# Performance work log

Measured on AMD Instinct MI355X. Metric: run time of the kernel, lower is better.

The kernel has to match this reference:

```python
import jax, jax.numpy as jnp
import numpy as np

D = 512; H = 8; DFF = 2048; S1 = 1024; S2 = 512; B = 8; EPS = 1e-5


def setup_inputs() -> dict:
    key = jax.random.key(0)
    ks = jax.random.split(key, 10)
    def w(k, shape):
        return jax.random.normal(k, shape, dtype=jnp.float32) * 0.02
    return {
        "rna_embed": jax.random.normal(ks[0], (S1, B, D), dtype=jnp.float32),
        "protein_embed": jax.random.normal(ks[1], (S2, B, D), dtype=jnp.float32),
        # self-attention params (torch MHA packed in_proj)
        "Wqkv_s": w(ks[2], (3 * D, D)), "bqkv_s": jnp.zeros((3 * D,), jnp.float32),
        "Wo_s": w(ks[3], (D, D)), "bo_s": jnp.zeros((D,), jnp.float32),
        # cross-attention params
        "Wqkv_c": w(ks[4], (3 * D, D)), "bqkv_c": jnp.zeros((3 * D,), jnp.float32),
        "Wo_c": w(ks[5], (D, D)), "bo_c": jnp.zeros((D,), jnp.float32),
        # FFN params
        "W1": w(ks[6], (DFF, D)), "b1": jnp.zeros((DFF,), jnp.float32),
        "W2": w(ks[7], (D, DFF)), "b2": jnp.zeros((D,), jnp.float32),
        # LayerNorm params: norm0_1, norm1_1, norm1_2, norm2
        "g0": jnp.ones((D,), jnp.float32), "be0": jnp.zeros((D,), jnp.float32),
        "g11": jnp.ones((D,), jnp.float32), "be11": jnp.zeros((D,), jnp.float32),
        "g12": jnp.ones((D,), jnp.float32), "be12": jnp.zeros((D,), jnp.float32),
        "g2": jnp.ones((D,), jnp.float32), "be2": jnp.zeros((D,), jnp.float32),
    }


def _layernorm(x, g, b):
    m = jnp.mean(x, axis=-1, keepdims=True)
    v = jnp.mean(jnp.square(x - m), axis=-1, keepdims=True)
    return (x - m) * jax.lax.rsqrt(v + EPS) * g + b


def _mha(xq, xkv, Wqkv, bqkv, Wo, bo):
    # xq: (Sq, B, D), xkv: (Sk, B, D)
    Wq, Wk, Wv = jnp.split(Wqkv, 3, axis=0)
    bq, bk, bv = jnp.split(bqkv, 3)
    hd = D // H
    scale = 1.0 / np.sqrt(hd).astype(np.float32)
    q = (xq @ Wq.T + bq).reshape(xq.shape[0], -1, H, hd)   # (Sq,B,H,hd)
    k = (xkv @ Wk.T + bk).reshape(xkv.shape[0], -1, H, hd)  # (Sk,B,H,hd)
    v = (xkv @ Wv.T + bv).reshape(xkv.shape[0], -1, H, hd)
    scores = jnp.einsum('qbhd,kbhd->bhqk', q, k) * scale    # (B,H,Sq,Sk)
    attn = jax.nn.softmax(scores, axis=-1)
    o = jnp.einsum('bhqk,kbhd->qbhd', attn, v).reshape(xq.shape[0], -1, D)
    return o @ Wo.T + bo


def reference(rna_embed, protein_embed, Wqkv_s, bqkv_s, Wo_s, bo_s,
              Wqkv_c, bqkv_c, Wo_c, bo_c, W1, b1, W2, b2,
              g0, be0, g11, be11, g12, be12, g2, be2):
    x1 = rna_embed
    # pre-norm self-attention
    h = _layernorm(x1, g0, be0)
    x1 = x1 + _mha(h, h, Wqkv_s, bqkv_s, Wo_s, bo_s)
    # pre-norm cross-attention (queries from x1, keys/values from protein)
    x1 = x1 + _mha(_layernorm(x1, g11, be11), _layernorm(protein_embed, g12, be12),
                   Wqkv_c, bqkv_c, Wo_c, bo_c)
    # pre-norm FFN
    h = _layernorm(x1, g2, be2)
    x1 = x1 + (jax.nn.relu(h @ W1.T + b1) @ W2.T + b2)
    return x1
```

## Files before the change

### kernel.cpp

```cpp
#include <hip/hip_runtime.h>

typedef unsigned short u16;
typedef unsigned int u32;
typedef u16 u16x8 __attribute__((ext_vector_type(8)));
typedef u16 u16x4 __attribute__((ext_vector_type(4)));
typedef short bfx8 __attribute__((ext_vector_type(8)));
typedef float f32x4 __attribute__((ext_vector_type(4)));

#define AS1 __attribute__((address_space(1)))
#define AS3 __attribute__((address_space(3)))

__device__ __forceinline__ u16 f2bf(float f) {
  union { float f; u32 u; } c; c.f = f;
  u32 u = c.u;
  u += 0x7fffu + ((u >> 16) & 1u);
  return (u16)(u >> 16);
}

__device__ __forceinline__ float bf2f(u16 b) {
  union { u32 u; float f; } c; c.u = ((u32)b) << 16;
  return c.f;
}

__device__ __forceinline__ u32 cvt_pk_bf16(float lo, float hi) {
  u32 r;
  asm("v_cvt_pk_bf16_f32 %0, %1, %2" : "=v"(r) : "v"(lo), "v"(hi));
  return r;
}

__device__ __forceinline__ float fexp2(float x) {
  float r;
  asm("v_exp_f32 %0, %1" : "=v"(r) : "v"(x));
  return r;
}

__device__ __forceinline__ void ln_core(float f[8], const float* __restrict__ g,
                                        const float* __restrict__ be,
                                        u16* __restrict__ out, int gw, int lane) {
  float s = 0.f, q = 0.f;
#pragma unroll
  for (int e = 0; e < 8; ++e) { s += f[e]; q += f[e] * f[e]; }
#pragma unroll
  for (int m = 1; m < 64; m <<= 1) { s += __shfl_xor(s, m); q += __shfl_xor(q, m); }
  float mean = s * (1.f / 512.f);
  float var = q * (1.f / 512.f) - mean * mean;
  float rs = rsqrtf(var + 1e-5f);
  const float4* g4 = (const float4*)g;
  const float4* b4 = (const float4*)be;
  float4 ga = g4[2 * lane], gb = g4[2 * lane + 1];
  float4 ba = b4[2 * lane], bb = b4[2 * lane + 1];
  float gv[8] = {ga.x, ga.y, ga.z, ga.w, gb.x, gb.y, gb.z, gb.w};
  float bv[8] = {ba.x, ba.y, ba.z, ba.w, bb.x, bb.y, bb.z, bb.w};
  u16x8 o;
#pragma unroll
  for (int e = 0; e < 8; ++e) o[e] = f2bf((f[e] - mean) * rs * gv[e] + bv[e]);
  ((u16x8*)(out + (size_t)gw * 512))[lane] = o;
}

__device__ __forceinline__ void ln_row_f32(const float* __restrict__ x, const float* __restrict__ g,
                                           const float* __restrict__ be, u16* __restrict__ out,
                                           int gw, int lane) {
  const float4* row = (const float4*)(x + (size_t)gw * 512);
  float4 a = row[2 * lane], b = row[2 * lane + 1];
  float f[8] = {a.x, a.y, a.z, a.w, b.x, b.y, b.z, b.w};
  ln_core(f, g, be, out, gw, lane);
}

__device__ __forceinline__ void ln_row_bf16(const u16* __restrict__ x, const float* __restrict__ g,
                                            const float* __restrict__ be, u16* __restrict__ out,
                                            int gw, int lane) {
  u16x8 v = ((const u16x8*)(x + (size_t)gw * 512))[lane];
  float f[8];
#pragma unroll
  for (int e = 0; e < 8; ++e) f[e] = bf2f(v[e]);
  ln_core(f, g, be, out, gw, lane);
}

__global__ __launch_bounds__(256) void cvtln_kernel(const float* __restrict__ a0, const float* __restrict__ a1,
                                                    const float* __restrict__ a2, const float* __restrict__ a3,
                                                    const float* __restrict__ a4, const float* __restrict__ a5,
                                                    u16* __restrict__ b0, u16* __restrict__ b1,
                                                    u16* __restrict__ b2, u16* __restrict__ b3,
                                                    u16* __restrict__ b4, u16* __restrict__ b5,
                                                    const float* __restrict__ x, const float* __restrict__ g,
                                                    const float* __restrict__ be, u16* __restrict__ lnout) {
  if (blockIdx.x < 4096) {
    int i = blockIdx.x * 256 + threadIdx.x;
    const float* s; u16* d; int off;
    if      (i < 196608) { s = a0; d = b0; off = i; }
    else if (i < 262144) { s = a1; d = b1; off = i - 196608; }
    else if (i < 458752) { s = a2; d = b2; off = i - 262144; }
    else if (i < 524288) { s = a3; d = b3; off = i - 458752; }
    else if (i < 786432) { s = a4; d = b4; off = i - 524288; }
    else                 { s = a5; d = b5; off = i - 786432; }
    float4 v = ((const float4*)s)[off];
    u16x4 o;
    o[0] = f2bf(v.x); o[1] = f2bf(v.y); o[2] = f2bf(v.z); o[3] = f2bf(v.w);
    ((u16x4*)d)[off] = o;
  } else {
    int gw = ((blockIdx.x - 4096) * 256 + threadIdx.x) >> 6;
    ln_row_f32(x, g, be, lnout, gw, threadIdx.x & 63);
  }
}

__global__ __launch_bounds__(256) void lnb_kernel(const u16* __restrict__ x,
                                                  const float* __restrict__ g,
                                                  const float* __restrict__ be,
                                                  u16* __restrict__ out, int ntok) {
  int gw = (blockIdx.x * 256 + threadIdx.x) >> 6;
  if (gw >= ntok) return;
  ln_row_bf16(x, g, be, out, gw, threadIdx.x & 63);
}

__global__ __launch_bounds__(256) void ln2_kernel(const u16* __restrict__ xa, const float* __restrict__ ga,
                                                  const float* __restrict__ ba, u16* __restrict__ oa,
                                                  const float* __restrict__ xb, const float* __restrict__ gb,
                                                  const float* __restrict__ bb, u16* __restrict__ ob) {
  int lane = threadIdx.x & 63;
  if (blockIdx.x < 2048) {
    int gw = (blockIdx.x * 256 + threadIdx.x) >> 6;
    ln_row_bf16(xa, ga, ba, oa, gw, lane);
  } else {
    int gw = ((blockIdx.x - 2048) * 256 + threadIdx.x) >> 6;
    ln_row_f32(xb, gb, bb, ob, gw, lane);
  }
}

__global__ __launch_bounds__(256) void vt_kernel(const u16* __restrict__ vB, u16* __restrict__ vt,
                                                 int stride, int S) {
  __shared__ u16 lt[64 * 68];
  const int t = threadIdx.x;
  const int b = blockIdx.y, h = blockIdx.z;
  const int sr = t >> 3, dc = (t & 7) * 8;
#pragma unroll
  for (int p = 0; p < 2; ++p) {
    int s = blockIdx.x * 64 + sr + p * 32;
    u16x8 v = *(const u16x8*)(vB + (size_t)(s * 8 + b) * stride + h * 64 + dc);
    u16x4 lo, hi;
    lo[0]=v[0]; lo[1]=v[1]; lo[2]=v[2]; lo[3]=v[3];
    hi[0]=v[4]; hi[1]=v[5]; hi[2]=v[6]; hi[3]=v[7];
    *(u16x4*)&lt[(sr + p * 32) * 68 + dc] = lo;
    *(u16x4*)&lt[(sr + p * 32) * 68 + dc + 4] = hi;
  }
  __syncthreads();
#pragma unroll
  for (int p = 0; p < 2; ++p) {
    int d = sr + p * 32;
    u16x8 o;
#pragma unroll
    for (int e = 0; e < 8; ++e) o[e] = lt[(dc + e) * 68 + d];
    *(u16x8*)(vt + ((size_t)(b * 8 + h) * 64 + d) * S + blockIdx.x * 64 + dc) = o;
  }
}

template <int EPI, int BM, int BN>
__device__ __forceinline__ void gemm8_body(const u16* __restrict__ A,
                                           const u16* __restrict__ Bw,
                                           const float* __restrict__ bias,
                                           const void* __restrict__ res,
                                           void* __restrict__ Cout,
                                           int M, int K, int bn, int bm) {
  constexpr int WCg = BN / 64;
  constexpr int WRg = 8 / WCg;
  constexpr int RPW = BM / WRg;
  constexpr int IM = RPW / 16;
  constexpr int LD = (BM + BN) / 64;
  __shared__ __align__(16) u16 lA[2][BM * 64];
  __shared__ __align__(16) u16 lB[2][BN * 64];
  const int tid = threadIdx.x;
  const int lane = tid & 63, w = tid >> 6;
  const int wr = w / WCg, wc = w % WCg;
  const int r15 = lane & 15, kg = lane >> 4;
  const int xr = (r15 & 7) << 4;

  f32x4 acc[IM][4] = {};

  const int lrw = tid >> 3;
  const int lcl = ((tid & 7) * 8) ^ ((lrw & 7) * 8);
  const u16* gA = A + (size_t)(bn + lrw) * K + lcl;
  const u16* gB = Bw + (size_t)(bm + lrw) * K + lcl;
  const int ldsbase = (w * 8) * 64;

#define STAGE8(buf, t) do {                                                               \
    _Pragma("unroll")                                                                     \
    for (int i_ = 0; i_ < BM / 64; ++i_)                                                  \
      __builtin_amdgcn_global_load_lds((AS1 u32*)(gA + (size_t)(i_ * 64) * K + (t) * 64), \
                                       (AS3 u32*)&lA[buf][i_ * 4096 + ldsbase], 16, 0, 0);\
    _Pragma("unroll")                                                                     \
    for (int i_ = 0; i_ < BN / 64; ++i_)                                                  \
      __builtin_amdgcn_global_load_lds((AS1 u32*)(gB + (size_t)(i_ * 64) * K + (t) * 64), \
                                       (AS3 u32*)&lB[buf][i_ * 4096 + ldsbase], 16, 0, 0);\
  } while (0)

  const int nk = K >> 6;
  STAGE8(0, 0);
  for (int t = 0; t < nk; ++t) {
    const int cur = t & 1;
    if (t + 1 < nk) {
      STAGE8(cur ^ 1, t + 1);
      if constexpr (LD == 3)      asm volatile("s_waitcnt vmcnt(3)" ::: "memory");
      else if constexpr (LD == 4) asm volatile("s_waitcnt vmcnt(4)" ::: "memory");
      else                        asm volatile("s_waitcnt vmcnt(8)" ::: "memory");
    } else {
      asm volatile("s_waitcnt vmcnt(0)" ::: "memory");
    }
    __builtin_amdgcn_sched_barrier(0);
    __builtin_amdgcn_s_barrier();
    __builtin_amdgcn_sched_barrier(0);

    const char* Ac = (const char*)lA[cur];
    const char* Bc = (const char*)lB[cur];
    __builtin_amdgcn_s_setprio(1);
#pragma unroll
    for (int kk = 0; kk < 2; ++kk) {
      bfx8 a[IM], b[4];
#pragma unroll
      for (int i = 0; i < IM; ++i)
        a[i] = *(const bfx8*)(Ac + (wr * RPW + i * 16 + r15) * 128 + ((kk * 64 + kg * 16) ^ xr));
#pragma unroll
      for (int j = 0; j < 4; ++j)
        b[j] = *(const bfx8*)(Bc + (wc * 64 + j * 16 + r15) * 128 + ((kk * 64 + kg * 16) ^ xr));
#pragma unroll
      for (int i = 0; i < IM; ++i)
#pragma unroll
        for (int j = 0; j < 4; ++j)
          acc[i][j] = __builtin_amdgcn_mfma_f32_16x16x32_bf16(a[i], b[j], acc[i][j], 0, 0, 0);
    }
    __builtin_amdgcn_s_setprio(0);
    __builtin_amdgcn_sched_barrier(0);
    __builtin_amdgcn_s_barrier();
  }
#undef STAGE8

#pragma unroll
  for (int i = 0; i < IM; ++i) {
#pragma unroll
    for (int j = 0; j < 4; ++j) {
      int col = bm + wc * 64 + j * 16 + r15;
      float bv = bias[col];
#pragma unroll
      for (int r = 0; r < 4; ++r) {
        int row = bn + wr * RPW + i * 16 + kg * 4 + r;
        size_t idx = (size_t)row * M + col;
        float v = acc[i][j][r] + bv;
        if (EPI == 1) v = fmaxf(v, 0.f);
        if (EPI == 3) {
          ((u16*)Cout)[idx] = f2bf(((const float*)res)[idx] + v);
        } else if (EPI == 4) {
          ((u16*)Cout)[idx] = f2bf(bf2f(((const u16*)res)[idx]) + v);
        } else if (EPI == 5) {
          ((float*)Cout)[idx] = bf2f(((const u16*)res)[idx]) + v;
        } else {
          ((u16*)Cout)[idx] = f2bf(v);
        }
      }
    }
  }
}

template <int EPI, int BM, int BN, int MINW>
__global__ __launch_bounds__(512, MINW) void gemm8(const u16* __restrict__ A,
                                                   const u16* __restrict__ Bw,
                                                   const float* __restrict__ bias,
                                                   const void* __restrict__ res,
                                                   void* __restrict__ Cout,
                                                   int N, int M, int K) {
  const int nwg = gridDim.x * gridDim.y;
  const int id = blockIdx.y * gridDim.x + blockIdx.x;
  const int swz = (id & 7) * (nwg >> 3) + (id >> 3);
  const int bn = (swz / gridDim.x) * BM;
  const int bm = (swz % gridDim.x) * BN;
  gemm8_body<EPI, BM, BN>(A, Bw, bias, res, Cout, M, K, bn, bm);
}

__global__ __launch_bounds__(512, 6) void gemm8_dual(const u16* __restrict__ A0, const u16* __restrict__ W0,
                                                     const float* __restrict__ c0, u16* __restrict__ O0,
                                                     const u16* __restrict__ A1, const u16* __restrict__ W1,
                                                     const float* __restrict__ c1, u16* __restrict__ O1) {
  const int id = blockIdx.x;
  const u16 *A, *Bw; const float* bias; u16* C; int M, gx, lid;
  if (id < 512) { A = A0; Bw = W0; bias = c0; C = O0; M = 512;  gx = 4; lid = id; }
  else          { A = A1; Bw = W1; bias = c1; C = O1; M = 1024; gx = 8; lid = id - 512; }
  const int swz = (lid & 7) * 64 + (lid >> 3);
  const int bn = (swz / gx) * 64;
  const int bm = (swz % gx) * 128;
  gemm8_body<0, 64, 128>(A, Bw, bias, nullptr, C, M, 512, bn, bm);
}

__global__ __launch_bounds__(512, 2) void attn_kernel(const u16* __restrict__ qB,
                                                      const u16* __restrict__ kB,
                                                      const u16* __restrict__ vtB,
                                                      u16* __restrict__ oB,
                                                      int qStride, int kvStride, int Sk) {
  __shared__ __align__(16) u16 lK[4][64 * 64];
  __shared__ __align__(16) u16 lVt[4][64 * 64];
  const int tid = threadIdx.x, lane = tid & 63, w = tid >> 6;
  const int sid = blockIdx.x;
  const int h = sid & 7, b = (sid >> 3) & 7, qt = sid >> 6;
  const int r15 = lane & 15, kg = lane >> 4;
  const int srow = lane >> 3;
  const int sxcol = ((lane & 7) * 8) ^ (srow * 8);

  const int q0 = qt * 256 + w * 32 + r15;
  const u16* qrow0 = qB + (size_t)(q0 * 8 + b) * qStride + h * 64;
  const u16* qrow1 = qB + (size_t)((q0 + 16) * 8 + b) * qStride + h * 64;
  bfx8 qf0a = *(const bfx8*)(qrow0 + kg * 8);
  bfx8 qf0b = *(const bfx8*)(qrow0 + 32 + kg * 8);
  bfx8 qf1a = *(const bfx8*)(qrow1 + kg * 8);
  bfx8 qf1b = *(const bfx8*)(qrow1 + 32 + kg * 8);

  const int rl = w * 8 + srow;
  const int krow = (rl & 32) | ((rl & 12) << 1) | ((rl & 16) >> 2) | (rl & 3);

  const u16* vbase = vtB + ((size_t)(b * 8 + h) * 64) * Sk;
  const u16* kp0 = kB + ((size_t)krow * 8 + b) * kvStride + h * 64 + sxcol;
  const size_t kAdv = (size_t)64 * 8 * kvStride;
  const u16* vp0 = vbase + (size_t)rl * Sk + sxcol;

#define STAGE(buf, tt) do {                                                           \
    __builtin_amdgcn_global_load_lds((AS1 u32*)(kp0 + (size_t)(tt) * kAdv),           \
                                     (AS3 u32*)&lK[buf][(w * 8) * 64], 16, 0, 0);     \
    __builtin_amdgcn_global_load_lds((AS1 u32*)(vp0 + (size_t)(tt) * 64),             \
                                     (AS3 u32*)&lVt[buf][(w * 8) * 64], 16, 0, 0);    \
  } while (0)

  const int nt = Sk / 64;
  const int np = nt >> 1;
  STAGE(0, 0); STAGE(1, 1);

  f32x4 oacc0[4] = {}, oacc1[4] = {};
  float mrow0 = -1e30f, mrow1 = -1e30f, lsum0 = 0.f, lsum1 = 0.f;
  const float C2 = 0.125f * 1.44269504088896340736f;
  const int xr = (r15 & 7) << 4;

  for (int i = 0; i < np; ++i) {
    __builtin_amdgcn_sched_barrier(0);
    __builtin_amdgcn_s_barrier();
    __builtin_amdgcn_sched_barrier(0);
    if (i + 1 < np) {
      const int sb = ((i + 1) & 1) * 2;
      STAGE(sb, 2 * (i + 1)); STAGE(sb + 1, 2 * (i + 1) + 1);
      asm volatile("s_waitcnt vmcnt(4)" ::: "memory");
    } else {
      asm volatile("s_waitcnt vmcnt(0)" ::: "memory");
    }
    __builtin_amdgcn_sched_barrier(0);

#pragma unroll
    for (int tb = 0; tb < 2; ++tb) {
      const int buf = (i & 1) * 2 + tb;
      const char* Kc = (const char*)lK[buf];
      const char* Vc = (const char*)lVt[buf];

      f32x4 s0[4] = {}, s1[4] = {};
      __builtin_amdgcn_s_setprio(1);
#pragma unroll
      for (int j = 0; j < 4; ++j) {
        const char* kp = Kc + (j * 16 + r15) * 128;
        bfx8 kf0 = *(const bfx8*)(kp + ((kg * 16) ^ xr));
        bfx8 kf1 = *(const bfx8*)(kp + ((64 + kg * 16) ^ xr));
        s0[j] = __builtin_amdgcn_mfma_f32_16x16x32_bf16(kf0, qf0a, s0[j], 0, 0, 0);
        s0[j] = __builtin_amdgcn_mfma_f32_16x16x32_bf16(kf1, qf0b, s0[j], 0, 0, 0);
        s1[j] = __builtin_amdgcn_mfma_f32_16x16x32_bf16(kf0, qf1a, s1[j], 0, 0, 0);
        s1[j] = __builtin_amdgcn_mfma_f32_16x16x32_bf16(kf1, qf1b, s1[j], 0, 0, 0);
      }
      __builtin_amdgcn_s_setprio(0);

      float lm0 = fmaxf(fmaxf(fmaxf(s0[0][0], s0[0][1]), fmaxf(s0[0][2], s0[0][3])),
                 fmaxf(fmaxf(fmaxf(s0[1][0], s0[1][1]), fmaxf(s0[1][2], s0[1][3])),
                 fmaxf(fmaxf(fmaxf(s0[2][0], s0[2][1]), fmaxf(s0[2][2], s0[2][3])),
                       fmaxf(fmaxf(s0[3][0], s0[3][1]), fmaxf(s0[3][2], s0[3][3])))));
      if (!__all(lm0 <= mrow0 + 16.0f)) {
        float m0 = fmaxf(lm0, __shfl_xor(lm0, 16));
        m0 = fmaxf(m0, __shfl_xor(m0, 32));
        float mn = fmaxf(mrow0, m0);
        float corr = fexp2((mrow0 - mn) * C2);
        mrow0 = mn;
        lsum0 *= corr;
#pragma unroll
        for (int jd = 0; jd < 4; ++jd)
#pragma unroll
          for (int r = 0; r < 4; ++r) oacc0[jd][r] *= corr;
      }
      float lm1 = fmaxf(fmaxf(fmaxf(s1[0][0], s1[0][1]), fmaxf(s1[0][2], s1[0][3])),
                 fmaxf(fmaxf(fmaxf(s1[1][0], s1[1][1]), fmaxf(s1[1][2], s1[1][3])),
                 fmaxf(fmaxf(fmaxf(s1[2][0], s1[2][1]), fmaxf(s1[2][2], s1[2][3])),
                       fmaxf(fmaxf(s1[3][0], s1[3][1]), fmaxf(s1[3][2], s1[3][3])))));
      if (!__all(lm1 <= mrow1 + 16.0f)) {
        float m1 = fmaxf(lm1, __shfl_xor(lm1, 16));
        m1 = fmaxf(m1, __shfl_xor(m1, 32));
        float mn = fmaxf(mrow1, m1);
        float corr = fexp2((mrow1 - mn) * C2);
        mrow1 = mn;
        lsum1 *= corr;
#pragma unroll
        for (int jd = 0; jd < 4; ++jd)
#pragma unroll
          for (int r = 0; r < 4; ++r) oacc1[jd][r] *= corr;
      }

      float bc0 = -mrow0 * C2, bc1 = -mrow1 * C2;
      float p0[4][4], p1[4][4];
      float ps0 = 0.f, ps1 = 0.f;
#pragma unroll
      for (int j = 0; j < 4; ++j)
#pragma unroll
        for (int r = 0; r < 4; ++r) {
          p0[j][r] = fexp2(fmaf(s0[j][r], C2, bc0));
          p1[j][r] = fexp2(fmaf(s1[j][r], C2, bc1));
          ps0 += p0[j][r]; ps1 += p1[j][r];
        }
      lsum0 += ps0; lsum1 += ps1;

      __builtin_amdgcn_s_setprio(1);
#pragma unroll
      for (int s2 = 0; s2 < 2; ++s2) {
        union { u32 u[4]; bfx8 v; } pt0, pt1;
        pt0.u[0] = cvt_pk_bf16(p0[2 * s2][0],     p0[2 * s2][1]);
        pt0.u[1] = cvt_pk_bf16(p0[2 * s2][2],     p0[2 * s2][3]);
        pt0.u[2] = cvt_pk_bf16(p0[2 * s2 + 1][0], p0[2 * s2 + 1][1]);
        pt0.u[3] = cvt_pk_bf16(p0[2 * s2 + 1][2], p0[2 * s2 + 1][3]);
        pt1.u[0] = cvt_pk_bf16(p1[2 * s2][0],     p1[2 * s2][1]);
        pt1.u[1] = cvt_pk_bf16(p1[2 * s2][2],     p1[2 * s2][3]);
        pt1.u[2] = cvt_pk_bf16(p1[2 * s2 + 1][0], p1[2 * s2 + 1][1]);
        pt1.u[3] = cvt_pk_bf16(p1[2 * s2 + 1][2], p1[2 * s2 + 1][3]);
#pragma unroll
        for (int jd = 0; jd < 4; ++jd) {
          const char* vp = Vc + (jd * 16 + r15) * 128;
          bfx8 vf = *(const bfx8*)(vp + ((s2 * 64 + kg * 16) ^ xr));
          oacc0[jd] = __builtin_amdgcn_mfma_f32_16x16x32_bf16(vf, pt0.v, oacc0[jd], 0, 0, 0);
          oacc1[jd] = __builtin_amdgcn_mfma_f32_16x16x32_bf16(vf, pt1.v, oacc1[jd], 0, 0, 0);
        }
      }
      __builtin_amdgcn_s_setprio(0);
    }
  }
#undef STAGE

  lsum0 += __shfl_xor(lsum0, 16);
  lsum0 += __shfl_xor(lsum0, 32);
  lsum1 += __shfl_xor(lsum1, 16);
  lsum1 += __shfl_xor(lsum1, 32);
  float inv0 = 1.f / lsum0, inv1 = 1.f / lsum1;
  u16* orow0 = oB + (size_t)(q0 * 8 + b) * 512 + h * 64;
  u16* orow1 = oB + (size_t)((q0 + 16) * 8 + b) * 512 + h * 64;
#pragma unroll
  for (int jd = 0; jd < 4; ++jd) {
    *(u32*)(orow0 + jd * 16 + kg * 4)     = cvt_pk_bf16(oacc0[jd][0] * inv0, oacc0[jd][1] * inv0);
    *(u32*)(orow0 + jd * 16 + kg * 4 + 2) = cvt_pk_bf16(oacc0[jd][2] * inv0, oacc0[jd][3] * inv0);
    *(u32*)(orow1 + jd * 16 + kg * 4)     = cvt_pk_bf16(oacc1[jd][0] * inv1, oacc1[jd][1] * inv1);
    *(u32*)(orow1 + jd * 16 + kg * 4 + 2) = cvt_pk_bf16(oacc1[jd][2] * inv1, oacc1[jd][3] * inv1);
  }
}

extern "C" void kernel_launch(void* const* d_in, const int* in_sizes, int n_in,
                              void* d_out, int out_size, void* d_ws, size_t ws_size,
                              hipStream_t stream) {
  const float* rna    = (const float*)d_in[0];
  const float* prot   = (const float*)d_in[1];
  const float* Wqkv_s = (const float*)d_in[2];
  const float* bqkv_s = (const float*)d_in[3];
  const float* Wo_s   = (const float*)d_in[4];
  const float* bo_s   = (const float*)d_in[5];
  const float* Wqkv_c = (const float*)d_in[6];
  const float* bqkv_c = (const float*)d_in[7];
  const float* Wo_c   = (const float*)d_in[8];
  const float* bo_c   = (const float*)d_in[9];
  const float* W1     = (const float*)d_in[10];
  const float* b1     = (const float*)d_in[11];
  const float* W2     = (const float*)d_in[12];
  const float* b2     = (const float*)d_in[13];
  const float* g0  = (const float*)d_in[14];
  const float* be0 = (const float*)d_in[15];
  const float* g11 = (const float*)d_in[16];
  const float* be11= (const float*)d_in[17];
  const float* g12 = (const float*)d_in[18];
  const float* be12= (const float*)d_in[19];
  const float* g2  = (const float*)d_in[20];
  const float* be2 = (const float*)d_in[21];
  float* out = (float*)d_out;

  u16* wbf      = (u16*)d_ws;
  u16* w_qkv_s  = wbf;
  u16* w_o_s    = wbf + 786432;
  u16* w_qkv_c  = wbf + 1048576;
  u16* w_o_c    = wbf + 1835008;
  u16* w_1      = wbf + 2097152;
  u16* w_2      = wbf + 3145728;
  u16* hbuf     = wbf + 4194304;
  u16* qkv      = hbuf + 4194304;
  u16* kvc      = qkv + 4194304;
  u16* attnO    = qkv + 12582912;
  u16* hp       = attnO + 4194304;
  u16* x1b      = hp + 2097152;
  u16* x1c      = x1b + 4194304;
  u16* ffnmid   = qkv;

  cvtln_kernel<<<6144, 256, 0, stream>>>(Wqkv_s, Wo_s, Wqkv_c, Wo_c, W1, W2,
                                         w_qkv_s, w_o_s, w_qkv_c, w_o_c, w_1, w_2,
                                         rna, g0, be0, hbuf);

  gemm8<0, 128, 128, 4><<<dim3(12, 64), 512, 0, stream>>>(hbuf, w_qkv_s, bqkv_s, nullptr, qkv, 8192, 1536, 512);
  vt_kernel<<<dim3(16, 8, 8), 256, 0, stream>>>(qkv + 1024, hbuf, 1536, 1024);
  attn_kernel<<<256, 512, 0, stream>>>(qkv, qkv + 512, hbuf, attnO, 1536, 1536, 1024);
  gemm8<3, 64, 128, 6><<<dim3(4, 128), 512, 0, stream>>>(attnO, w_o_s, bo_s, rna, x1b, 8192, 512, 512);

  ln2_kernel<<<3072, 256, 0, stream>>>(x1b, g11, be11, hbuf, prot, g12, be12, hp);
  gemm8_dual<<<1024, 512, 0, stream>>>(hbuf, w_qkv_c, bqkv_c, qkv,
                                       hp, w_qkv_c + 512 * 512, bqkv_c + 512, kvc);
  vt_kernel<<<dim3(8, 8, 8), 256, 0, stream>>>(kvc + 512, hp, 1024, 512);
  attn_kernel<<<256, 512, 0, stream>>>(qkv, kvc, hp, attnO, 512, 1024, 512);
  gemm8<4, 64, 128, 6><<<dim3(4, 128), 512, 0, stream>>>(attnO, w_o_c, bo_c, x1b, x1c, 8192, 512, 512);

  lnb_kernel<<<2048, 256, 0, stream>>>(x1c, g2, be2, hbuf, 8192);
  gemm8<1, 128, 128, 4><<<dim3(16, 64), 512, 0, stream>>>(hbuf, w_1, b1, nullptr, ffnmid, 8192, 2048, 512);
  gemm8<5, 64, 128, 6><<<dim3(4, 128), 512, 0, stream>>>(ffnmid, w_2, b2, x1c, out, 8192, 512, 2048);
}
```

Measured before the change: 188.0 us.

## Hoist protein LN and cross K/V projection into early fused kernels

```diff
diff --git a/kernel.cpp b/kernel.cpp
--- a/kernel.cpp
+++ b/kernel.cpp
@@ -83,7 +83,9 @@
                                                     u16* __restrict__ b2, u16* __restrict__ b3,
                                                     u16* __restrict__ b4, u16* __restrict__ b5,
                                                     const float* __restrict__ x, const float* __restrict__ g,
-                                                    const float* __restrict__ be, u16* __restrict__ lnout) {
+                                                    const float* __restrict__ be, u16* __restrict__ lnout,
+                                                    const float* __restrict__ xp, const float* __restrict__ gp,
+                                                    const float* __restrict__ bep, u16* __restrict__ lnoutp) {
   if (blockIdx.x < 4096) {
     int i = blockIdx.x * 256 + threadIdx.x;
     const float* s; u16* d; int off;
@@ -97,9 +99,12 @@
     u16x4 o;
     o[0] = f2bf(v.x); o[1] = f2bf(v.y); o[2] = f2bf(v.z); o[3] = f2bf(v.w);
     ((u16x4*)d)[off] = o;
-  } else {
+  } else if (blockIdx.x < 6144) {
     int gw = ((blockIdx.x - 4096) * 256 + threadIdx.x) >> 6;
     ln_row_f32(x, g, be, lnout, gw, threadIdx.x & 63);
+  } else {
+    int gw = ((blockIdx.x - 6144) * 256 + threadIdx.x) >> 6;
+    ln_row_f32(xp, gp, bep, lnoutp, gw, threadIdx.x & 63);
   }
 }
 
@@ -112,29 +117,14 @@
   ln_row_bf16(x, g, be, out, gw, threadIdx.x & 63);
 }
 
-__global__ __launch_bounds__(256) void ln2_kernel(const u16* __restrict__ xa, const float* __restrict__ ga,
-                                                  const float* __restrict__ ba, u16* __restrict__ oa,
-                                                  const float* __restrict__ xb, const float* __restrict__ gb,
-                                                  const float* __restrict__ bb, u16* __restrict__ ob) {
-  int lane = threadIdx.x & 63;
-  if (blockIdx.x < 2048) {
-    int gw = (blockIdx.x * 256 + threadIdx.x) >> 6;
-    ln_row_bf16(xa, ga, ba, oa, gw, lane);
-  } else {
-    int gw = ((blockIdx.x - 2048) * 256 + threadIdx.x) >> 6;
-    ln_row_f32(xb, gb, bb, ob, gw, lane);
-  }
-}
-
-__global__ __launch_bounds__(256) void vt_kernel(const u16* __restrict__ vB, u16* __restrict__ vt,
-                                                 int stride, int S) {
+__device__ __forceinline__ void vt_body(const u16* __restrict__ vB, u16* __restrict__ vt,
+                                        int stride, int S, int xblk, int b, int h) {
   __shared__ u16 lt[64 * 68];
   const int t = threadIdx.x;
-  const int b = blockIdx.y, h = blockIdx.z;
   const int sr = t >> 3, dc = (t & 7) * 8;
 #pragma unroll
   for (int p = 0; p < 2; ++p) {
-    int s = blockIdx.x * 64 + sr + p * 32;
+    int s = xblk * 64 + sr + p * 32;
     u16x8 v = *(const u16x8*)(vB + (size_t)(s * 8 + b) * stride + h * 64 + dc);
     u16x4 lo, hi;
     lo[0]=v[0]; lo[1]=v[1]; lo[2]=v[2]; lo[3]=v[3];
@@ -149,31 +139,44 @@
     u16x8 o;
 #pragma unroll
     for (int e = 0; e < 8; ++e) o[e] = lt[(dc + e) * 68 + d];
-    *(u16x8*)(vt + ((size_t)(b * 8 + h) * 64 + d) * S + blockIdx.x * 64 + dc) = o;
-  }
-}
-
-template <int EPI, int BM, int BN>
+    *(u16x8*)(vt + ((size_t)(b * 8 + h) * 64 + d) * S + xblk * 64 + dc) = o;
+  }
+}
+
+__global__ __launch_bounds__(256) void vt2_kernel(const u16* __restrict__ v0, u16* __restrict__ t0,
+                                                  const u16* __restrict__ v1, u16* __restrict__ t1) {
+  int id = blockIdx.x;
+  if (id < 1024) {
+    vt_body(v0, t0, 1536, 1024, id & 15, (id >> 4) & 7, id >> 7);
+  } else {
+    int l = id - 1024;
+    vt_body(v1, t1, 1024, 512, l & 7, (l >> 3) & 7, l >> 6);
+  }
+}
+
+template <int EPI, int BM, int BN, int WRg>
 __device__ __forceinline__ void gemm8_body(const u16* __restrict__ A,
                                            const u16* __restrict__ Bw,
                                            const float* __restrict__ bias,
                                            const void* __restrict__ res,
                                            void* __restrict__ Cout,
-                                           int M, int K, int bn, int bm) {
-  constexpr int WCg = BN / 64;
-  constexpr int WRg = 8 / WCg;
+                                           int M, int K, int bn, int bm,
+                                           u16* __restrict__ lds) {
+  constexpr int WCg = 8 / WRg;
   constexpr int RPW = BM / WRg;
   constexpr int IM = RPW / 16;
+  constexpr int CPW = BN / WCg;
+  constexpr int JN = CPW / 16;
   constexpr int LD = (BM + BN) / 64;
-  __shared__ __align__(16) u16 lA[2][BM * 64];
-  __shared__ __align__(16) u16 lB[2][BN * 64];
+  u16* lA = lds;
+  u16* lB = lds + 2 * BM * 64;
   const int tid = threadIdx.x;
   const int lane = tid & 63, w = tid >> 6;
   const int wr = w / WCg, wc = w % WCg;
   const int r15 = lane & 15, kg = lane >> 4;
   const int xr = (r15 & 7) << 4;
 
-  f32x4 acc[IM][4] = {};
+  f32x4 acc[IM][JN] = {};
 
   const int lrw = tid >> 3;
   const int lcl = ((tid & 7) * 8) ^ ((lrw & 7) * 8);
@@ -185,11 +188,11 @@
     _Pragma("unroll")                                                                     \
     for (int i_ = 0; i_ < BM / 64; ++i_)                                                  \
       __builtin_amdgcn_global_load_lds((AS1 u32*)(gA + (size_t)(i_ * 64) * K + (t) * 64), \
-                                       (AS3 u32*)&lA[buf][i_ * 4096 + ldsbase], 16, 0, 0);\
+                                       (AS3 u32*)&lA[(buf) * BM * 64 + i_ * 4096 + ldsbase], 16, 0, 0);\
     _Pragma("unroll")                                                                     \
     for (int i_ = 0; i_ < BN / 64; ++i_)                                                  \
       __builtin_amdgcn_global_load_lds((AS1 u32*)(gB + (size_t)(i_ * 64) * K + (t) * 64), \
-                                       (AS3 u32*)&lB[buf][i_ * 4096 + ldsbase], 16, 0, 0);\
+                                       (AS3 u32*)&lB[(buf) * BN * 64 + i_ * 4096 + ldsbase], 16, 0, 0);\
   } while (0)
 
   const int nk = K >> 6;
@@ -208,22 +211,22 @@
     __builtin_amdgcn_s_barrier();
     __builtin_amdgcn_sched_barrier(0);
 
-    const char* Ac = (const char*)lA[cur];
-    const char* Bc = (const char*)lB[cur];
+    const char* Ac = (const char*)&lA[cur * BM * 64];
+    const char* Bc = (const char*)&lB[cur * BN * 64];
     __builtin_amdgcn_s_setprio(1);
 #pragma unroll
     for (int kk = 0; kk < 2; ++kk) {
-      bfx8 a[IM], b[4];
+      bfx8 a[IM], b[JN];
 #pragma unroll
       for (int i = 0; i < IM; ++i)
         a[i] = *(const bfx8*)(Ac + (wr * RPW + i * 16 + r15) * 128 + ((kk * 64 + kg * 16) ^ xr));
 #pragma unroll
-      for (int j = 0; j < 4; ++j)
-        b[j] = *(const bfx8*)(Bc + (wc * 64 + j * 16 + r15) * 128 + ((kk * 64 + kg * 16) ^ xr));
+      for (int j = 0; j < JN; ++j)
+        b[j] = *(const bfx8*)(Bc + (wc * CPW + j * 16 + r15) * 128 + ((kk * 64 + kg * 16) ^ xr));
 #pragma unroll
       for (int i = 0; i < IM; ++i)
 #pragma unroll
-        for (int j = 0; j < 4; ++j)
+        for (int j = 0; j < JN; ++j)
           acc[i][j] = __builtin_amdgcn_mfma_f32_16x16x32_bf16(a[i], b[j], acc[i][j], 0, 0, 0);
     }
     __builtin_amdgcn_s_setprio(0);
@@ -235,8 +238,8 @@
 #pragma unroll
   for (int i = 0; i < IM; ++i) {
 #pragma unroll
-    for (int j = 0; j < 4; ++j) {
-      int col = bm + wc * 64 + j * 16 + r15;
+    for (int j = 0; j < JN; ++j) {
+      int col = bm + wc * CPW + j * 16 + r15;
       float bv = bias[col];
 #pragma unroll
       for (int r = 0; r < 4; ++r) {
@@ -258,33 +261,38 @@
   }
 }
 
-template <int EPI, int BM, int BN, int MINW>
+template <int EPI, int BM, int BN, int WRg, int MINW>
 __global__ __launch_bounds__(512, MINW) void gemm8(const u16* __restrict__ A,
                                                    const u16* __restrict__ Bw,
                                                    const float* __restrict__ bias,
                                                    const void* __restrict__ res,
                                                    void* __restrict__ Cout,
                                                    int N, int M, int K) {
+  __shared__ __align__(16) u16 lds[2 * (BM + BN) * 64];
   const int nwg = gridDim.x * gridDim.y;
   const int id = blockIdx.y * gridDim.x + blockIdx.x;
   const int swz = (id & 7) * (nwg >> 3) + (id >> 3);
   const int bn = (swz / gridDim.x) * BM;
   const int bm = (swz % gridDim.x) * BN;
-  gemm8_body<EPI, BM, BN>(A, Bw, bias, res, Cout, M, K, bn, bm);
-}
-
-__global__ __launch_bounds__(512, 6) void gemm8_dual(const u16* __restrict__ A0, const u16* __restrict__ W0,
+  gemm8_body<EPI, BM, BN, WRg>(A, Bw, bias, res, Cout, M, K, bn, bm, lds);
+}
+
+__global__ __launch_bounds__(512, 4) void gemm_qkvkv(const u16* __restrict__ A0, const u16* __restrict__ W0,
                                                      const float* __restrict__ c0, u16* __restrict__ O0,
                                                      const u16* __restrict__ A1, const u16* __restrict__ W1,
                                                      const float* __restrict__ c1, u16* __restrict__ O1) {
+  __shared__ __align__(16) u16 lds[2 * 256 * 64];
   const int id = blockIdx.x;
-  const u16 *A, *Bw; const float* bias; u16* C; int M, gx, lid;
-  if (id < 512) { A = A0; Bw = W0; bias = c0; C = O0; M = 512;  gx = 4; lid = id; }
-  else          { A = A1; Bw = W1; bias = c1; C = O1; M = 1024; gx = 8; lid = id - 512; }
-  const int swz = (lid & 7) * 64 + (lid >> 3);
-  const int bn = (swz / gx) * 64;
-  const int bm = (swz % gx) * 128;
-  gemm8_body<0, 64, 128>(A, Bw, bias, nullptr, C, M, 512, bn, bm);
+  if (id < 768) {
+    const int swz = (id & 7) * 96 + (id >> 3);
+    gemm8_body<0, 128, 128, 4>(A0, W0, c0, nullptr, O0, 1536, 512,
+                               (swz / 12) * 128, (swz % 12) * 128, lds);
+  } else {
+    const int lid = id - 768;
+    const int swz = (lid & 7) * 64 + (lid >> 3);
+    gemm8_body<0, 64, 128, 2>(A1, W1, c1, nullptr, O1, 1024, 512,
+                              (swz / 8) * 64, (swz % 8) * 128, lds);
+  }
 }
 
 __global__ __launch_bounds__(512, 2) void attn_kernel(const u16* __restrict__ qB,
@@ -496,23 +504,24 @@
   u16* x1c      = x1b + 4194304;
   u16* ffnmid   = qkv;
 
-  cvtln_kernel<<<6144, 256, 0, stream>>>(Wqkv_s, Wo_s, Wqkv_c, Wo_c, W1, W2,
+  cvtln_kernel<<<7168, 256, 0, stream>>>(Wqkv_s, Wo_s, Wqkv_c, Wo_c, W1, W2,
                                          w_qkv_s, w_o_s, w_qkv_c, w_o_c, w_1, w_2,
-                                         rna, g0, be0, hbuf);
-
-  gemm8<0, 128, 128, 4><<<dim3(12, 64), 512, 0, stream>>>(hbuf, w_qkv_s, bqkv_s, nullptr, qkv, 8192, 1536, 512);
-  vt_kernel<<<dim3(16, 8, 8), 256, 0, stream>>>(qkv + 1024, hbuf, 1536, 1024);
+                                         rna, g0, be0, hbuf, prot, g12, be12, hp);
+
+  gemm_qkvkv<<<1280, 512, 0, stream>>>(hbuf, w_qkv_s, bqkv_s, qkv,
+                                       hp, w_qkv_c + 512 * 512, bqkv_c + 512, kvc);
+
+  vt2_kernel<<<1536, 256, 0, stream>>>(qkv + 1024, hbuf, kvc + 512, hp);
+
   attn_kernel<<<256, 512, 0, stream>>>(qkv, qkv + 512, hbuf, attnO, 1536, 1536, 1024);
-  gemm8<3, 64, 128, 6><<<dim3(4, 128), 512, 0, stream>>>(attnO, w_o_s, bo_s, rna, x1b, 8192, 512, 512);
-
-  ln2_kernel<<<3072, 256, 0, stream>>>(x1b, g11, be11, hbuf, prot, g12, be12, hp);
-  gemm8_dual<<<1024, 512, 0, stream>>>(hbuf, w_qkv_c, bqkv_c, qkv,
-                                       hp, w_qkv_c + 512 * 512, bqkv_c + 512, kvc);
-  vt_kernel<<<dim3(8, 8, 8), 256, 0, stream>>>(kvc + 512, hp, 1024, 512);
+  gemm8<3, 64, 128, 2, 6><<<dim3(4, 128), 512, 0, stream>>>(attnO, w_o_s, bo_s, rna, x1b, 8192, 512, 512);
+
+  lnb_kernel<<<2048, 256, 0, stream>>>(x1b, g11, be11, hbuf, 8192);
+  gemm8<0, 64, 128, 2, 6><<<dim3(4, 128), 512, 0, stream>>>(hbuf, w_qkv_c, bqkv_c, nullptr, qkv, 8192, 512, 512);
   attn_kernel<<<256, 512, 0, stream>>>(qkv, kvc, hp, attnO, 512, 1024, 512);
-  gemm8<4, 64, 128, 6><<<dim3(4, 128), 512, 0, stream>>>(attnO, w_o_c, bo_c, x1b, x1c, 8192, 512, 512);
+  gemm8<4, 64, 128, 2, 6><<<dim3(4, 128), 512, 0, stream>>>(attnO, w_o_c, bo_c, x1b, x1c, 8192, 512, 512);
 
   lnb_kernel<<<2048, 256, 0, stream>>>(x1c, g2, be2, hbuf, 8192);
-  gemm8<1, 128, 128, 4><<<dim3(16, 64), 512, 0, stream>>>(hbuf, w_1, b1, nullptr, ffnmid, 8192, 2048, 512);
-  gemm8<5, 64, 128, 6><<<dim3(4, 128), 512, 0, stream>>>(ffnmid, w_2, b2, x1c, out, 8192, 512, 2048);
-}
+  gemm8<1, 128, 128, 4, 4><<<dim3(16, 64), 512, 0, stream>>>(hbuf, w_1, b1, nullptr, ffnmid, 8192, 2048, 512);
+  gemm8<5, 64, 128, 2, 6><<<dim3(4, 128), 512, 0, stream>>>(ffnmid, w_2, b2, x1c, out, 8192, 512, 2048);
+}
```

New measurement: 174.0 us, median of 3. 7.5% less time.
